# Kernel tuning notes

Hardware: AMD Instinct MI355X
Metric: run time of the kernel (lower is better)

## Reference

```python
import jax, jax.numpy as jnp
import numpy as np

EMBED = 512
INPUT = 512
NEGINF = -1000000.0


def setup_inputs() -> dict:
    key = jax.random.key(0)
    k1, k2, k3, k4, k5, k6, k7 = jax.random.split(key, 7)
    B, S = 8, 2048
    return {
        "Xin_q": jax.random.normal(k1, (B, S, INPUT), dtype=jnp.float32),
        "Xin_k": jax.random.normal(k2, (B, S, INPUT), dtype=jnp.float32),
        "Xin_v": jax.random.normal(k3, (B, S, INPUT), dtype=jnp.float32),
        "mask": jax.random.randint(k4, (B, S, S), 0, 2, dtype=jnp.int32),
        # Linear weights stored as (input, embed) so projection is x @ W
        "Wq": jax.random.normal(k5, (INPUT, EMBED), dtype=jnp.float32) / np.sqrt(INPUT),
        "Wk": jax.random.normal(k6, (INPUT, EMBED), dtype=jnp.float32) / np.sqrt(INPUT),
        "Wv": jax.random.normal(k7, (INPUT, EMBED), dtype=jnp.float32) / np.sqrt(INPUT),
    }


def reference(Xin_q, Xin_k, Xin_v, mask, Wq, Wk, Wv):
    scale = EMBED ** 0.25  # each of Q and K divided by d^(1/4) -> QK^T / sqrt(d)
    Xq = (Xin_q @ Wq) / scale          # [B,S,E]
    Xk = (Xin_k @ Wk) / scale          # [B,S,E]
    Xv = Xin_v @ Wv                    # [B,S,E]
    attn_w = jnp.einsum("bqe,bke->bqk", Xq, Xk)  # [B,S,S]
    attn_w = jnp.where(mask == 0, NEGINF, attn_w)
    attn_p = jax.nn.softmax(attn_w, axis=2)
    # post-softmax unnormalized mask-multiply (nonstandard)
    attn_p = attn_p * mask.astype(attn_p.dtype)
    z = jnp.einsum("bqk,bke->bqe", attn_p, Xv)   # [B,S,E]
    return (z, attn_p)
```

## Files before the change

### kernel.cpp

```cpp
#include <hip/hip_runtime.h>
#include <stdint.h>

typedef __attribute__((ext_vector_type(8))) short short8;
typedef __attribute__((ext_vector_type(4))) float f32x4;
typedef __attribute__((ext_vector_type(4))) int i32x4;
typedef __attribute__((ext_vector_type(8))) unsigned short ushort8v;

#define NEGINF_F (-1000000.0f)
#define MFMA16 __builtin_amdgcn_mfma_f32_16x16x32_bf16

__device__ __forceinline__ unsigned short f2bf(float f) {
  union { float f; uint32_t u; } v; v.f = f;
  uint32_t r = (v.u + 0x7FFFu + ((v.u >> 16) & 1u)) >> 16;
  return (unsigned short)r;
}
__device__ __forceinline__ void gl_lds16(const void* g, void* l) {
  __builtin_amdgcn_global_load_lds(
      (const __attribute__((address_space(1))) void*)g,
      (__attribute__((address_space(3))) void*)l, 16, 0, 0);
}
#define BARRIER() asm volatile("s_barrier" ::: "memory")

__global__ __launch_bounds__(512, 1)
void gemm256(const unsigned short* __restrict__ A,
             const unsigned short* __restrict__ B,
             float* __restrict__ C, const int* __restrict__ mask,
             int K, int lda, int ldb, int ldc,
             long sA, long sB, long sC, long sM)
{
  __shared__ __align__(16) unsigned short lds[65536];

  const int t = threadIdx.x;
  const int b = blockIdx.z;
  const unsigned short* Ap = A + (long)b * sA;
  const unsigned short* Bp = B + (long)b * sB;
  const int* mp = mask + (long)b * sM;
  const int tm = blockIdx.x * 256;
  const int tn = blockIdx.y * 256;

  const int lane = t & 63, wave = t >> 6;
  const int wm = (wave >> 2) * 128;
  const int wn = (wave & 3) * 64;
  const int q = lane >> 4, mr = lane & 15;

  f32x4 acc[8][4];
#pragma unroll
  for (int m = 0; m < 8; m++)
#pragma unroll
    for (int n = 0; n < 4; n++) acc[m][n] = (f32x4){0.f, 0.f, 0.f, 0.f};

  const int srow = t >> 2;
  const int scol = (t & 3) * 8;

  auto stage = [&](int kt) {
    unsigned short* L = lds + (kt & 3) * 16384;
    const int k0 = kt << 5;
    const unsigned short* ga = Ap + (long)(tm + srow) * lda + k0 + scol;
    gl_lds16(ga,                  L + (size_t)t * 8);
    gl_lds16(ga + (long)128 * lda, L + 4096 + (size_t)t * 8);
    const unsigned short* gb = Bp + (long)(tn + srow) * ldb + k0 + scol;
    gl_lds16(gb,                  L + 8192 + (size_t)t * 8);
    gl_lds16(gb + (long)128 * ldb, L + 12288 + (size_t)t * 8);
  };

  auto compute = [&](int kt) {
    const unsigned short* LA = lds + (kt & 3) * 16384;
    const unsigned short* LB = LA + 8192;
    short8 af[8], b0, b1;
#pragma unroll
    for (int m = 0; m < 8; m++)
      af[m] = *(const short8*)&LA[(size_t)(wm + m * 16 + mr) * 32 + q * 8];
    b0 = *(const short8*)&LB[(size_t)(wn + 0 * 16 + mr) * 32 + q * 8];
    b1 = *(const short8*)&LB[(size_t)(wn + 1 * 16 + mr) * 32 + q * 8];
    __builtin_amdgcn_s_setprio(1);
#pragma unroll
    for (int m = 0; m < 8; m++) acc[m][0] = MFMA16(af[m], b0, acc[m][0], 0, 0, 0);
#pragma unroll
    for (int m = 0; m < 8; m++) acc[m][1] = MFMA16(af[m], b1, acc[m][1], 0, 0, 0);
    __builtin_amdgcn_s_setprio(0);
    BARRIER();
    b0 = *(const short8*)&LB[(size_t)(wn + 2 * 16 + mr) * 32 + q * 8];
    b1 = *(const short8*)&LB[(size_t)(wn + 3 * 16 + mr) * 32 + q * 8];
    __builtin_amdgcn_s_setprio(1);
#pragma unroll
    for (int m = 0; m < 8; m++) acc[m][2] = MFMA16(af[m], b0, acc[m][2], 0, 0, 0);
#pragma unroll
    for (int m = 0; m < 8; m++) acc[m][3] = MFMA16(af[m], b1, acc[m][3], 0, 0, 0);
    __builtin_amdgcn_s_setprio(0);
  };

  const int NT = K >> 5;
  stage(0); stage(1); stage(2);

  for (int kt = 0; kt < NT - 3; ++kt) {
    stage(kt + 3);
    asm volatile("s_waitcnt vmcnt(12)" ::: "memory");
    BARRIER();
    compute(kt);
    BARRIER();
  }
  asm volatile("s_waitcnt vmcnt(8)" ::: "memory");
  BARRIER(); compute(NT - 3); BARRIER();
  asm volatile("s_waitcnt vmcnt(4)" ::: "memory");
  BARRIER(); compute(NT - 2); BARRIER();
  asm volatile("s_waitcnt vmcnt(0)" ::: "memory");
  BARRIER(); compute(NT - 1);

  float* co = C + (long)b * sC;
#pragma unroll
  for (int m = 0; m < 8; m++) {
#pragma unroll
    for (int n = 0; n < 4; n++) {
      const int row0 = tm + wm + m * 16 + q * 4;
      const int col  = tn + wn + n * 16 + mr;
#pragma unroll
      for (int r = 0; r < 4; r++) {
        float x = acc[m][n][r];
        const long idx = (long)(row0 + r) * ldc + col;
        if (!mp[idx]) x = NEGINF_F;
        co[idx] = x;
      }
    }
  }
}

template<bool A32, bool OUT32, bool MASKED>
__global__ __launch_bounds__(256, A32 ? 2 : 4)
void gemm_nt(const void* __restrict__ Av, const unsigned short* __restrict__ B,
             void* __restrict__ Cv, const int* __restrict__ mask,
             int K, int lda, int ldb, int ldc,
             long sA, long sB, long sC, long sM, float scale)
{
  constexpr int ABYTES = A32 ? 128 * 32 * 4 : 128 * 32 * 2;
  constexpr int BBYTES = 128 * 32 * 2;
  constexpr int BUFB = ABYTES + BBYTES;
  __shared__ __align__(16) unsigned char smem[2 * BUFB];

  const int t = threadIdx.x;
  const int b = blockIdx.z;
  const float* Af = (const float*)Av + (long)b * sA;
  const unsigned short* Ah = (const unsigned short*)Av + (long)b * sA;
  const unsigned short* Bp = B + (long)b * sB;
  const int* mp = MASKED ? (mask + (long)b * sM) : nullptr;
  const int tm = blockIdx.x * 128;
  const int tn = blockIdx.y * 128;

  const int lane = t & 63, wave = t >> 6;
  const int wm = (wave & 1) * 64, wn = (wave >> 1) * 64;
  const int q = lane >> 4, mr = lane & 15;

  f32x4 acc[4][4];
#pragma unroll
  for (int i = 0; i < 4; i++)
#pragma unroll
    for (int j = 0; j < 4; j++) acc[i][j] = (f32x4){0.f, 0.f, 0.f, 0.f};

  const int r0a = t >> 2;
  const int cswz = ((t & 3) ^ ((t >> 2) & 3)) * 8;
  const int sw8 = (q ^ (mr & 3)) * 8;

  auto stage = [&](int buf, int k0) {
    unsigned char* base = smem + buf * BUFB;
    if (A32) {
      float* Asf = (float*)base;
#pragma unroll
      for (int rd = 0; rd < 4; rd++) {
        const int f = rd * 1024 + t * 4;
        const int row = f >> 5, col = f & 31;
        gl_lds16(Af + (long)(tm + row) * lda + k0 + col, Asf + f);
      }
    } else {
      unsigned short* Ash = (unsigned short*)base;
      const unsigned short* ga = Ah + (long)(tm + r0a) * lda + k0 + cswz;
      gl_lds16(ga, &Ash[(size_t)t * 8]);
      gl_lds16(ga + (long)64 * lda, &Ash[(size_t)(t + 256) * 8]);
    }
    unsigned short* Bsb = (unsigned short*)(base + ABYTES);
    const unsigned short* gb = Bp + (long)(tn + r0a) * ldb + k0 + cswz;
    gl_lds16(gb, &Bsb[(size_t)t * 8]);
    gl_lds16(gb + (long)64 * ldb, &Bsb[(size_t)(t + 256) * 8]);
  };

  const int nt = K >> 5;
  stage(0, 0);
  __syncthreads();

  for (int ti = 0; ti < nt; ++ti) {
    if (ti + 1 < nt) stage((ti + 1) & 1, (ti + 1) << 5);

    const unsigned char* base = smem + (ti & 1) * BUFB;
    const unsigned short* Bs = (const unsigned short*)(base + ABYTES);
    short8 af[4], bfr[4];
#pragma unroll
    for (int i = 0; i < 4; i++) {
      if (A32) {
        const float* Asf = (const float*)base;
        const int fb = (wm + i * 16 + mr) * 32 + q * 8;
        const f32x4 x0 = *(const f32x4*)&Asf[fb];
        const f32x4 x1 = *(const f32x4*)&Asf[fb + 4];
        short8 v;
        v[0] = (short)f2bf(x0[0]); v[1] = (short)f2bf(x0[1]);
        v[2] = (short)f2bf(x0[2]); v[3] = (short)f2bf(x0[3]);
        v[4] = (short)f2bf(x1[0]); v[5] = (short)f2bf(x1[1]);
        v[6] = (short)f2bf(x1[2]); v[7] = (short)f2bf(x1[3]);
        af[i] = v;
      } else {
        const unsigned short* Ash = (const unsigned short*)base;
        af[i] = *(const short8*)&Ash[(size_t)(wm + i * 16 + mr) * 32 + sw8];
      }
      bfr[i] = *(const short8*)&Bs[(size_t)(wn + i * 16 + mr) * 32 + sw8];
    }
#pragma unroll
    for (int i = 0; i < 4; i++)
#pragma unroll
      for (int j = 0; j < 4; j++)
        acc[i][j] = MFMA16(af[i], bfr[j], acc[i][j], 0, 0, 0);

    if (ti + 1 < nt) __syncthreads();
  }

  if (OUT32) {
    float* ep = (float*)smem;
    float* co = (float*)Cv + (long)b * sC;
    const int band = wm >> 2;
    const int tr = t >> 3;
    const int tcb = (t & 7) * 16;
    const int growb = tm + (tr >> 4) * 64 + (tr & 15);
#pragma unroll
    for (int i = 0; i < 4; i++) {
      __syncthreads();
#pragma unroll
      for (int j = 0; j < 4; j++) {
        const int colb = wn + j * 16 + mr;
#pragma unroll
        for (int r = 0; r < 4; r++) {
          const int lr = band + q * 4 + r;
          ep[lr * 128 + ((colb + lr * 4) & 127)] = acc[i][j][r];
        }
      }
      __syncthreads();
      const int gr = growb + i * 16;
      const long rbase = (long)gr * ldc;
      const float* eprow = ep + tr * 128;
      const int rot = tr * 4;
#pragma unroll
      for (int k = 0; k < 4; k++) {
        const int lc = tcb + k * 4;
        f32x4 x = *(const f32x4*)&eprow[(lc + rot) & 127];
        x *= scale;
        if (MASKED) {
          const i32x4 mv = *(const i32x4*)&mp[rbase + tn + lc];
#pragma unroll
          for (int e = 0; e < 4; e++)
            if (!mv[e]) x[e] = NEGINF_F;
        }
        *(f32x4*)&co[rbase + tn + lc] = x;
      }
    }
  } else {
#pragma unroll
    for (int i = 0; i < 4; i++) {
#pragma unroll
      for (int j = 0; j < 4; j++) {
        const int row0 = tm + wm + i * 16 + q * 4;
        const int col  = tn + wn + j * 16 + mr;
        const f32x4 v = acc[i][j];
#pragma unroll
        for (int r = 0; r < 4; r++) {
          float x = v[r] * scale;
          ((unsigned short*)Cv + (long)b * sC)[(long)(row0 + r) * ldc + col] = f2bf(x);
        }
      }
    }
  }
}

__global__ __launch_bounds__(256) void softmax_rows_f32(
    float* __restrict__ P, unsigned short* __restrict__ Pb)
{
  const int row = blockIdx.x;
  float* p = P + (size_t)row * 2048;
  const int t = threadIdx.x, lane = t & 63, wv = t >> 6;
  f32x4 a = *(const f32x4*)(p + t * 8);
  f32x4 c = *(const f32x4*)(p + t * 8 + 4);
  float x[8] = {a[0], a[1], a[2], a[3], c[0], c[1], c[2], c[3]};
  float mx = x[0];
#pragma unroll
  for (int j = 1; j < 8; j++) mx = fmaxf(mx, x[j]);
#pragma unroll
  for (int o = 32; o > 0; o >>= 1) mx = fmaxf(mx, __shfl_xor(mx, o));
  __shared__ float rm[4], rs[4];
  if (lane == 0) rm[wv] = mx;
  __syncthreads();
  mx = fmaxf(fmaxf(rm[0], rm[1]), fmaxf(rm[2], rm[3]));
  float e[8], s = 0.f;
#pragma unroll
  for (int j = 0; j < 8; j++) { e[j] = __expf(x[j] - mx); s += e[j]; }
#pragma unroll
  for (int o = 32; o > 0; o >>= 1) s += __shfl_xor(s, o);
  if (lane == 0) rs[wv] = s;
  __syncthreads();
  s = rs[0] + rs[1] + rs[2] + rs[3];
  const float linv = (mx < -1.0e5f) ? 0.f : 1.f / s;
  f32x4 o0 = {e[0] * linv, e[1] * linv, e[2] * linv, e[3] * linv};
  f32x4 o1 = {e[4] * linv, e[5] * linv, e[6] * linv, e[7] * linv};
  *(f32x4*)(p + t * 8) = o0;
  *(f32x4*)(p + t * 8 + 4) = o1;
  if (Pb) {
    ushort8v ob;
    ob[0] = f2bf(o0[0]); ob[1] = f2bf(o0[1]); ob[2] = f2bf(o0[2]); ob[3] = f2bf(o0[3]);
    ob[4] = f2bf(o1[0]); ob[5] = f2bf(o1[1]); ob[6] = f2bf(o1[2]); ob[7] = f2bf(o1[3]);
    *(ushort8v*)(Pb + (size_t)row * 2048 + t * 8) = ob;
  }
}

__global__ __launch_bounds__(256) void cvt3(
    const float* __restrict__ s0, unsigned short* __restrict__ d0,
    const float* __restrict__ s1, unsigned short* __restrict__ d1,
    const float* __restrict__ s2, unsigned short* __restrict__ d2)
{
  const float* s = blockIdx.y == 0 ? s0 : (blockIdx.y == 1 ? s1 : s2);
  unsigned short* d = blockIdx.y == 0 ? d0 : (blockIdx.y == 1 ? d1 : d2);
  const size_t i = ((size_t)blockIdx.x * 256 + threadIdx.x) * 8;
  const float4 a = *(const float4*)(s + i);
  const float4 b = *(const float4*)(s + i + 4);
  ushort8v o;
  o[0] = f2bf(a.x); o[1] = f2bf(a.y); o[2] = f2bf(a.z); o[3] = f2bf(a.w);
  o[4] = f2bf(b.x); o[5] = f2bf(b.y); o[6] = f2bf(b.z); o[7] = f2bf(b.w);
  *(ushort8v*)(d + i) = o;
}

__global__ __launch_bounds__(256) void cvt_t_v(
    const float* __restrict__ src, unsigned short* __restrict__ dst)
{
  const int b = blockIdx.z;
  __shared__ float tile[32][33];
  const int s0 = blockIdx.x * 32, i0 = blockIdx.y * 32;
  const int tx = threadIdx.x & 31, ty = threadIdx.x >> 5;
#pragma unroll
  for (int r = 0; r < 4; r++) {
    const int srow = ty + r * 8;
    tile[srow][tx] = src[((size_t)b * 2048 + s0 + srow) * 512 + i0 + tx];
  }
  __syncthreads();
#pragma unroll
  for (int r = 0; r < 4; r++) {
    const int irow = ty + r * 8;
    dst[((size_t)b * 512 + i0 + irow) * 2048 + s0 + tx] = f2bf(tile[tx][irow]);
  }
}

__global__ __launch_bounds__(256) void transpose_w(
    const float* __restrict__ W0, const float* __restrict__ W1,
    const float* __restrict__ W2,
    unsigned short* __restrict__ T0, unsigned short* __restrict__ T1,
    unsigned short* __restrict__ T2)
{
  const float* W = blockIdx.z == 0 ? W0 : (blockIdx.z == 1 ? W1 : W2);
  unsigned short* T = blockIdx.z == 0 ? T0 : (blockIdx.z == 1 ? T1 : T2);
  __shared__ float tile[32][33];
  const int bx = blockIdx.x * 32, by = blockIdx.y * 32;
  const int tx = threadIdx.x & 31, ty = threadIdx.x >> 5;
#pragma unroll
  for (int i = 0; i < 4; i++) {
    const int r = ty + i * 8;
    tile[r][tx] = W[(size_t)(by + r) * 512 + bx + tx];
  }
  __syncthreads();
#pragma unroll
  for (int i = 0; i < 4; i++) {
    const int r = ty + i * 8;
    T[(size_t)(bx + r) * 512 + by + tx] = f2bf(tile[tx][r]);
  }
}

extern "C" void kernel_launch(void* const* d_in, const int* in_sizes, int n_in,
                              void* d_out, int out_size, void* d_ws, size_t ws_size,
                              hipStream_t stream) {
  const float* Xq = (const float*)d_in[0];
  const float* Xk = (const float*)d_in[1];
  const float* Xv = (const float*)d_in[2];
  const int*   mk = (const int*)d_in[3];
  const float* Wq = (const float*)d_in[4];
  const float* Wk = (const float*)d_in[5];
  const float* Wv = (const float*)d_in[6];

  float* z = (float*)d_out;
  float* P = z + (size_t)8 * 2048 * 512;

  unsigned short* w    = (unsigned short*)d_ws;
  unsigned short* Wtq  = w;
  unsigned short* Wtk  = w + 262144;
  unsigned short* Wtv  = w + 524288;
  unsigned short* buf1 = w + 786432;
  unsigned short* buf2 = buf1 + 8388608;
  unsigned short* Ks   = buf2 + 8388608;
  unsigned short* Pb   = Ks;
  const bool use_pb = ws_size >= (size_t)102236160;

  unsigned short* Xkb = (unsigned short*)P;
  unsigned short* Xvb = (unsigned short*)z;

  const float inv_scale = 0.21022410381342863f;

  transpose_w<<<dim3(16, 16, 3), 256, 0, stream>>>(Wq, Wk, Wv, Wtq, Wtk, Wtv);

  cvt3<<<dim3(4096, 3), 256, 0, stream>>>(Xq, buf1, Xk, Xkb, Xv, Xvb);

  gemm_nt<false, false, false><<<dim3(128, 4, 1), 256, 0, stream>>>(
      buf1, Wtq, buf2, nullptr, 512, 512, 512, 512, 0, 0, 0, 0, inv_scale);

  gemm_nt<false, false, false><<<dim3(128, 4, 1), 256, 0, stream>>>(
      Xkb, Wtk, Ks, nullptr, 512, 512, 512, 512, 0, 0, 0, 0, inv_scale);

  gemm256<<<dim3(8, 8, 8), 512, 0, stream>>>(
      buf2, Ks, P, mk, 512, 512, 512, 2048,
      1048576, 1048576, 4194304, 4194304);

  softmax_rows_f32<<<dim3(16384), 256, 0, stream>>>(P, use_pb ? Pb : nullptr);

  if (use_pb) {
    gemm_nt<false, false, false><<<dim3(4, 16, 8), 256, 0, stream>>>(
        Wtv, Xvb, buf2, nullptr, 512, 512, 512, 2048,
        0, 1048576, 1048576, 0, 1.0f);
    gemm_nt<false, true, false><<<dim3(16, 4, 8), 256, 0, stream>>>(
        Pb, buf2, z, nullptr, 2048, 2048, 2048, 512,
        4194304, 1048576, 1048576, 0, 1.0f);
  } else {
    cvt_t_v<<<dim3(64, 16, 8), 256, 0, stream>>>(Xv, buf1);
    gemm_nt<true, false, false><<<dim3(16, 4, 8), 256, 0, stream>>>(
        P, buf1, buf2, nullptr, 2048, 2048, 2048, 512,
        4194304, 1048576, 1048576, 0, 1.0f);
    gemm_nt<false, true, false><<<dim3(128, 4, 1), 256, 0, stream>>>(
        buf2, Wtv, z, nullptr, 512, 512, 512, 512, 0, 0, 0, 0, 1.0f);
  }
}
```

Measured before the change: 523.6 us.

## Use 256x256 gemm kernel for projections and PV, with an LDS-staged epilogue

Templates the 256x256 gemm kernel on mask and output type and uses it for the Q/K projections, merged into one batched launch, and for the V projection and P@V, replacing the 128x128 kernel. The mainloop changes from a 3-ahead prefetch to a 2-ahead prefetch, with A and B staged separately between MFMA halves. The fp32 masked score output now goes through an LDS-rotated buffer for coalesced vector stores and mask loads. The aim is more data reuse per block, fewer launches, and cheaper score writes. Raising launch bounds to 2 blocks per CU with 128 KB of LDS and 128 accumulator registers per thread risks register spills, and two blocks cannot both fit in LDS.

```diff
diff --git a/kernel.cpp b/kernel.cpp
--- a/kernel.cpp
+++ b/kernel.cpp
@@ -21,20 +21,21 @@
 }
 #define BARRIER() asm volatile("s_barrier" ::: "memory")
 
-__global__ __launch_bounds__(512, 1)
+template<bool MASKED, bool OUT32>
+__global__ __launch_bounds__(512, 2)
 void gemm256(const unsigned short* __restrict__ A,
              const unsigned short* __restrict__ B,
-             float* __restrict__ C, const int* __restrict__ mask,
+             void* __restrict__ Cv, const int* __restrict__ mask,
              int K, int lda, int ldb, int ldc,
-             long sA, long sB, long sC, long sM)
-{
-  __shared__ __align__(16) unsigned short lds[65536];
+             long sA, long sB, long sC, long sM, float scale)
+{
+  __shared__ __align__(16) unsigned short lds[4][16384];
 
   const int t = threadIdx.x;
   const int b = blockIdx.z;
   const unsigned short* Ap = A + (long)b * sA;
   const unsigned short* Bp = B + (long)b * sB;
-  const int* mp = mask + (long)b * sM;
+  const int* mp = MASKED ? (mask + (long)b * sM) : nullptr;
   const int tm = blockIdx.x * 256;
   const int tn = blockIdx.y * 256;
 
@@ -52,19 +53,26 @@
   const int srow = t >> 2;
   const int scol = (t & 3) * 8;
 
-  auto stage = [&](int kt) {
-    unsigned short* L = lds + (kt & 3) * 16384;
-    const int k0 = kt << 5;
-    const unsigned short* ga = Ap + (long)(tm + srow) * lda + k0 + scol;
-    gl_lds16(ga,                  L + (size_t)t * 8);
+  auto stage_a = [&](int kt) {
+    unsigned short* L = &lds[kt & 3][0];
+    const unsigned short* ga = Ap + (long)(tm + srow) * lda + (kt << 5) + scol;
+    gl_lds16(ga,                   L + (size_t)t * 8);
     gl_lds16(ga + (long)128 * lda, L + 4096 + (size_t)t * 8);
-    const unsigned short* gb = Bp + (long)(tn + srow) * ldb + k0 + scol;
-    gl_lds16(gb,                  L + 8192 + (size_t)t * 8);
-    gl_lds16(gb + (long)128 * ldb, L + 12288 + (size_t)t * 8);
   };
-
-  auto compute = [&](int kt) {
-    const unsigned short* LA = lds + (kt & 3) * 16384;
+  auto stage_b = [&](int kt) {
+    unsigned short* L = &lds[kt & 3][0] + 8192;
+    const unsigned short* gb = Bp + (long)(tn + srow) * ldb + (kt << 5) + scol;
+    gl_lds16(gb,                   L + (size_t)t * 8);
+    gl_lds16(gb + (long)128 * ldb, L + 4096 + (size_t)t * 8);
+  };
+
+  const int NT = K >> 5;
+  stage_a(0); stage_b(0); stage_a(1); stage_b(1);
+  asm volatile("s_waitcnt vmcnt(4)" ::: "memory");
+  BARRIER();
+
+  for (int kt = 0; kt < NT; ++kt) {
+    const unsigned short* LA = &lds[kt & 3][0];
     const unsigned short* LB = LA + 8192;
     short8 af[8], b0, b1;
 #pragma unroll
@@ -72,6 +80,8 @@
       af[m] = *(const short8*)&LA[(size_t)(wm + m * 16 + mr) * 32 + q * 8];
     b0 = *(const short8*)&LB[(size_t)(wn + 0 * 16 + mr) * 32 + q * 8];
     b1 = *(const short8*)&LB[(size_t)(wn + 1 * 16 + mr) * 32 + q * 8];
+    if (kt + 2 < NT) stage_a(kt + 2);
+    BARRIER();
     __builtin_amdgcn_s_setprio(1);
 #pragma unroll
     for (int m = 0; m < 8; m++) acc[m][0] = MFMA16(af[m], b0, acc[m][0], 0, 0, 0);
@@ -81,55 +91,81 @@
     BARRIER();
     b0 = *(const short8*)&LB[(size_t)(wn + 2 * 16 + mr) * 32 + q * 8];
     b1 = *(const short8*)&LB[(size_t)(wn + 3 * 16 + mr) * 32 + q * 8];
+    if (kt + 2 < NT) stage_b(kt + 2);
+    BARRIER();
     __builtin_amdgcn_s_setprio(1);
 #pragma unroll
     for (int m = 0; m < 8; m++) acc[m][2] = MFMA16(af[m], b0, acc[m][2], 0, 0, 0);
 #pragma unroll
     for (int m = 0; m < 8; m++) acc[m][3] = MFMA16(af[m], b1, acc[m][3], 0, 0, 0);
     __builtin_amdgcn_s_setprio(0);
-  };
-
-  const int NT = K >> 5;
-  stage(0); stage(1); stage(2);
-
-  for (int kt = 0; kt < NT - 3; ++kt) {
-    stage(kt + 3);
-    asm volatile("s_waitcnt vmcnt(12)" ::: "memory");
-    BARRIER();
-    compute(kt);
-    BARRIER();
-  }
-  asm volatile("s_waitcnt vmcnt(8)" ::: "memory");
-  BARRIER(); compute(NT - 3); BARRIER();
-  asm volatile("s_waitcnt vmcnt(4)" ::: "memory");
-  BARRIER(); compute(NT - 2); BARRIER();
-  asm volatile("s_waitcnt vmcnt(0)" ::: "memory");
-  BARRIER(); compute(NT - 1);
-
-  float* co = C + (long)b * sC;
-#pragma unroll
-  for (int m = 0; m < 8; m++) {
-#pragma unroll
-    for (int n = 0; n < 4; n++) {
-      const int row0 = tm + wm + m * 16 + q * 4;
-      const int col  = tn + wn + n * 16 + mr;
-#pragma unroll
-      for (int r = 0; r < 4; r++) {
-        float x = acc[m][n][r];
-        const long idx = (long)(row0 + r) * ldc + col;
-        if (!mp[idx]) x = NEGINF_F;
-        co[idx] = x;
-      }
-    }
-  }
-}
-
-template<bool A32, bool OUT32, bool MASKED>
+    if (kt + 1 < NT) {
+      if (kt + 2 < NT) asm volatile("s_waitcnt vmcnt(4)" ::: "memory");
+      else             asm volatile("s_waitcnt vmcnt(0)" ::: "memory");
+      BARRIER();
+    }
+  }
+
+  if (OUT32) {
+    float* ep = (float*)&lds[0][0];
+    float* co = (float*)Cv + (long)b * sC;
+    const int myh = wave >> 2;
+    const int tr = t >> 2;
+    const int cb = (t & 3) * 64;
+#pragma unroll
+    for (int h = 0; h < 2; h++) {
+      __syncthreads();
+      if (myh == h) {
+#pragma unroll
+        for (int m = 0; m < 8; m++)
+#pragma unroll
+          for (int n = 0; n < 4; n++)
+#pragma unroll
+            for (int r = 0; r < 4; r++) {
+              const int lr = m * 16 + q * 4 + r;
+              const int colr = (wn + n * 16 + mr + lr * 4) & 255;
+              ep[lr * 256 + colr] = acc[m][n][r] * scale;
+            }
+      }
+      __syncthreads();
+      const int grow = tm + h * 128 + tr;
+      const long rb = (long)grow * ldc + tn;
+      const float* eprow = ep + tr * 256;
+      const int rot = tr * 4;
+#pragma unroll
+      for (int j = 0; j < 16; j++) {
+        const int LC = cb + j * 4;
+        f32x4 x = *(const f32x4*)&eprow[(LC + rot) & 255];
+        if (MASKED) {
+          const i32x4 mv = *(const i32x4*)&mp[rb + LC];
+#pragma unroll
+          for (int e = 0; e < 4; e++)
+            if (!mv[e]) x[e] = NEGINF_F;
+        }
+        *(f32x4*)&co[rb + LC] = x;
+      }
+    }
+  } else {
+    unsigned short* co = (unsigned short*)Cv + (long)b * sC;
+#pragma unroll
+    for (int m = 0; m < 8; m++)
+#pragma unroll
+      for (int n = 0; n < 4; n++) {
+        const int row0 = tm + wm + m * 16 + q * 4;
+        const int col  = tn + wn + n * 16 + mr;
+#pragma unroll
+        for (int r = 0; r < 4; r++)
+          co[(long)(row0 + r) * ldc + col] = f2bf(acc[m][n][r] * scale);
+      }
+  }
+}
+
+template<bool A32, bool OUT32>
 __global__ __launch_bounds__(256, A32 ? 2 : 4)
 void gemm_nt(const void* __restrict__ Av, const unsigned short* __restrict__ B,
-             void* __restrict__ Cv, const int* __restrict__ mask,
+             void* __restrict__ Cv,
              int K, int lda, int ldb, int ldc,
-             long sA, long sB, long sC, long sM, float scale)
+             long sA, long sB, long sC, float scale)
 {
   constexpr int ABYTES = A32 ? 128 * 32 * 4 : 128 * 32 * 2;
   constexpr int BBYTES = 128 * 32 * 2;
@@ -141,7 +177,6 @@
   const float* Af = (const float*)Av + (long)b * sA;
   const unsigned short* Ah = (const unsigned short*)Av + (long)b * sA;
   const unsigned short* Bp = B + (long)b * sB;
-  const int* mp = MASKED ? (mask + (long)b * sM) : nullptr;
   const int tm = blockIdx.x * 128;
   const int tn = blockIdx.y * 128;
 
@@ -248,12 +283,6 @@
         const int lc = tcb + k * 4;
         f32x4 x = *(const f32x4*)&eprow[(lc + rot) & 127];
         x *= scale;
-        if (MASKED) {
-          const i32x4 mv = *(const i32x4*)&mp[rbase + tn + lc];
-#pragma unroll
-          for (int e = 0; e < 4; e++)
-            if (!mv[e]) x[e] = NEGINF_F;
-        }
         *(f32x4*)&co[rbase + tn + lc] = x;
       }
     }
@@ -278,8 +307,8 @@
 __global__ __launch_bounds__(256) void softmax_rows_f32(
     float* __restrict__ P, unsigned short* __restrict__ Pb)
 {
-  const int row = blockIdx.x;
-  float* p = P + (size_t)row * 2048;
+  const size_t row = blockIdx.x;
+  float* p = P + row * 2048;
   const int t = threadIdx.x, lane = t & 63, wv = t >> 6;
   f32x4 a = *(const f32x4*)(p + t * 8);
   f32x4 c = *(const f32x4*)(p + t * 8 + 4);
@@ -310,7 +339,7 @@
     ushort8v ob;
     ob[0] = f2bf(o0[0]); ob[1] = f2bf(o0[1]); ob[2] = f2bf(o0[2]); ob[3] = f2bf(o0[3]);
     ob[4] = f2bf(o1[0]); ob[5] = f2bf(o1[1]); ob[6] = f2bf(o1[2]); ob[7] = f2bf(o1[3]);
-    *(ushort8v*)(Pb + (size_t)row * 2048 + t * 8) = ob;
+    *(ushort8v*)(Pb + row * 2048 + t * 8) = ob;
   }
 }
 
@@ -390,48 +419,44 @@
 
   unsigned short* w    = (unsigned short*)d_ws;
   unsigned short* Wtq  = w;
-  unsigned short* Wtk  = w + 262144;
   unsigned short* Wtv  = w + 524288;
   unsigned short* buf1 = w + 786432;
   unsigned short* buf2 = buf1 + 8388608;
-  unsigned short* Ks   = buf2 + 8388608;
-  unsigned short* Pb   = Ks;
+  unsigned short* Pb   = buf2 + 8388608;
   const bool use_pb = ws_size >= (size_t)102236160;
 
-  unsigned short* Xkb = (unsigned short*)P;
-  unsigned short* Xvb = (unsigned short*)z;
+  unsigned short* Xqkb = (unsigned short*)P;
+  unsigned short* Xvb  = (unsigned short*)z;
 
   const float inv_scale = 0.21022410381342863f;
 
-  transpose_w<<<dim3(16, 16, 3), 256, 0, stream>>>(Wq, Wk, Wv, Wtq, Wtk, Wtv);
-
-  cvt3<<<dim3(4096, 3), 256, 0, stream>>>(Xq, buf1, Xk, Xkb, Xv, Xvb);
-
-  gemm_nt<false, false, false><<<dim3(128, 4, 1), 256, 0, stream>>>(
-      buf1, Wtq, buf2, nullptr, 512, 512, 512, 512, 0, 0, 0, 0, inv_scale);
-
-  gemm_nt<false, false, false><<<dim3(128, 4, 1), 256, 0, stream>>>(
-      Xkb, Wtk, Ks, nullptr, 512, 512, 512, 512, 0, 0, 0, 0, inv_scale);
-
-  gemm256<<<dim3(8, 8, 8), 512, 0, stream>>>(
-      buf2, Ks, P, mk, 512, 512, 512, 2048,
-      1048576, 1048576, 4194304, 4194304);
+  transpose_w<<<dim3(16, 16, 3), 256, 0, stream>>>(Wq, Wk, Wv, Wtq, Wtq + 262144, Wtv);
+
+  cvt3<<<dim3(4096, 3), 256, 0, stream>>>(Xq, Xqkb, Xk, Xqkb + 8388608, Xv, Xvb);
+
+  gemm256<false, false><<<dim3(64, 2, 2), 512, 0, stream>>>(
+      Xqkb, Wtq, buf1, nullptr, 512, 512, 512, 512,
+      8388608, 262144, 8388608, 0, inv_scale);
+
+  gemm256<true, true><<<dim3(8, 8, 8), 512, 0, stream>>>(
+      buf1, buf2, P, mk, 512, 512, 512, 2048,
+      1048576, 1048576, 4194304, 4194304, 1.0f);
 
   softmax_rows_f32<<<dim3(16384), 256, 0, stream>>>(P, use_pb ? Pb : nullptr);
 
   if (use_pb) {
-    gemm_nt<false, false, false><<<dim3(4, 16, 8), 256, 0, stream>>>(
-        Wtv, Xvb, buf2, nullptr, 512, 512, 512, 2048,
+    gemm256<false, false><<<dim3(2, 8, 8), 512, 0, stream>>>(
+        Wtv, Xvb, buf1, nullptr, 512, 512, 512, 2048,
         0, 1048576, 1048576, 0, 1.0f);
-    gemm_nt<false, true, false><<<dim3(16, 4, 8), 256, 0, stream>>>(
-        Pb, buf2, z, nullptr, 2048, 2048, 2048, 512,
+    gemm256<false, true><<<dim3(8, 2, 8), 512, 0, stream>>>(
+        Pb, buf1, z, nullptr, 2048, 2048, 2048, 512,
         4194304, 1048576, 1048576, 0, 1.0f);
   } else {
     cvt_t_v<<<dim3(64, 16, 8), 256, 0, stream>>>(Xv, buf1);
-    gemm_nt<true, false, false><<<dim3(16, 4, 8), 256, 0, stream>>>(
-        P, buf1, buf2, nullptr, 2048, 2048, 2048, 512,
-        4194304, 1048576, 1048576, 0, 1.0f);
-    gemm_nt<false, true, false><<<dim3(128, 4, 1), 256, 0, stream>>>(
-        buf2, Wtv, z, nullptr, 512, 512, 512, 512, 0, 0, 0, 0, 1.0f);
-  }
-}
+    gemm_nt<true, false><<<dim3(16, 4, 8), 256, 0, stream>>>(
+        P, buf1, buf2, 2048, 2048, 2048, 512,
+        4194304, 1048576, 1048576, 1.0f);
+    gemm_nt<false, true><<<dim3(128, 4, 1), 256, 0, stream>>>(
+        buf2, Wtv, z, 512, 512, 512, 512, 0, 0, 0, 1.0f);
+  }
+}
```

Measured after the change: 564.7 us. +7.9%, slower.
